# Kernel tuning notes

Hardware: AMD Instinct MI355X
Metric: run time of the kernel (lower is better)

## Reference

```python
import jax, jax.numpy as jnp
import numpy as np
import math

DIM = 512      # vMF embedding dim
B = 512        # batch
K = 10         # sample_size
C = 8192       # num_classes
L = 0.7        # kappa_confidence
T_REJ = 32     # fixed rejection-sampling tries (acceptance ~0.7 per try)


def _vmf_logc(k, dim=DIM):
    # Approximate log normalizer from the paper (approximate_logc=True path).
    nm14 = (dim - 1) / 4.0
    nm12 = (dim - 1) / 2.0
    np12 = (dim + 1) / 2.0
    sqrtm = jnp.sqrt(nm12 * nm12 + k * k)
    sqrtp = jnp.sqrt(np12 * np12 + k * k)
    return nm14 * (jnp.log(nm12 + sqrtm) + jnp.log(nm12 + sqrtp)) - 0.5 * (sqrtm + sqrtp)


def _split(params):
    # params layout: [log_probs(1), means(DIM), hidden_ik(1)] (single component).
    means = params[..., 1:1 + DIM]
    hidden_ik = params[..., -1]
    mu = means / jnp.linalg.norm(means, axis=-1, keepdims=True)
    kappa = 1.0 / jnp.exp(hidden_ik)  # positive(x) = exp(x) parametrization
    return mu, kappa


def _vmf_sample(key, mu, kappa, n):
    # Wood's algorithm, vectorized over (b, n) with fixed-count rejection.
    b, d = mu.shape
    kap = kappa[:, None]  # (b,1)
    bb = (-2.0 * kap + jnp.sqrt(4.0 * kap * kap + (d - 1) ** 2)) / (d - 1)
    x0 = (1.0 - bb) / (1.0 + bb)
    cc = kap * x0 + (d - 1) * jnp.log(1.0 - x0 * x0)
    kz, ku, kv = jax.random.split(key, 3)
    z = jax.random.beta(kz, (d - 1) / 2.0, (d - 1) / 2.0, (T_REJ, b, n))
    w = (1.0 - (1.0 + bb) * z) / (1.0 - (1.0 - bb) * z)  # (T,b,n)
    u = jax.random.uniform(ku, (T_REJ, b, n), minval=1e-10)
    acc = kap * w + (d - 1) * jnp.log(1.0 - x0 * w) - cc >= jnp.log(u)
    idx = jnp.argmax(acc, axis=0)  # first accepted try
    w_sel = jnp.take_along_axis(w, idx[None], axis=0)[0]  # (b,n)
    v = jax.random.normal(kv, (b, n, d))
    v = v - jnp.einsum('bnd,bd->bn', v, mu)[..., None] * mu[:, None, :]
    v = v / jnp.linalg.norm(v, axis=-1, keepdims=True)
    sin_t = jnp.sqrt(jnp.clip(1.0 - w_sel * w_sel, 0.0))
    return w_sel[..., None] * mu[:, None, :] + sin_t[..., None] * v  # (b,n,d)


def setup_inputs() -> dict:
    key = jax.random.key(0)
    kp, kw, kl = jax.random.split(key, 3)
    # Input distribution parameters: random means, hidden_ik ~ log(1/kappa) with realistic kappa.
    parameters = jax.random.normal(kp, (B, DIM + 2), dtype=jnp.float32)
    kappa0 = L / (1.0 - L * L) * (DIM - 1) / math.sqrt(DIM)  # ~31
    parameters = parameters.at[:, -1].set(0.1 * parameters[:, -1] - math.log(kappa0))
    # Class weight, built exactly as in __init__ (non-deterministic target).
    means = jax.random.normal(kw, (C, DIM), dtype=jnp.float32) * (L / (1.0 - L * L) * (DIM - 1) / math.sqrt(DIM))
    norm = jnp.linalg.norm(means, axis=-1, keepdims=True)
    hidden_ik = jnp.log(1.0 / norm)  # ipositive = log
    weight = jnp.concatenate([jnp.zeros((C, 1), jnp.float32), means, hidden_ik], axis=-1)
    log_scale = jnp.asarray(2.773, dtype=jnp.float32)
    labels = jax.random.randint(kl, (B,), 0, C)
    return {"parameters": parameters, "weight": weight, "log_scale": log_scale, "labels": labels}


def reference(parameters, weight, log_scale, labels):
    scale = jnp.exp(log_scale)
    mu_x, kappa_x = _split(parameters)   # (b,d), (b,)
    mu_w, kappa_w = _split(weight)       # (c,d), (c,)
    sample = _vmf_sample(jax.random.key(42), mu_x, kappa_x, K)  # (b,K,d)
    sample = sample / jnp.linalg.norm(sample, axis=-1, keepdims=True)
    # logmls(b,k,c): samples have concentration k1=scale; since all means are unit,
    # ||k1*m1 + k2*m2|| = sqrt(k1^2 + k2^2 + 2*k1*k2*cos) -> single GEMM over d.
    cos = jnp.einsum('bkd,cd->bkc', sample, mu_w)
    k1 = scale
    k2 = kappa_w
    kk = jnp.sqrt(k1 * k1 + k2 * k2 + 2.0 * k1 * (k2 * cos))  # (b,K,c)
    logmls = _vmf_logc(k1) + _vmf_logc(k2)[None, None, :] - _vmf_logc(kk)
    neg_logden = jax.scipy.special.logsumexp(logmls, axis=2) - _vmf_logc(scale)  # (b,K)
    neg_lognum = scale * jnp.einsum('bd,bd->b', mu_x, mu_w[labels])
    losses = neg_logden.mean(axis=1) - neg_lognum  # (b,)
    b = parameters.shape[0]
    logits = jnp.zeros((b, C), parameters.dtype).at[jnp.arange(b), labels].set(-losses)
    return logits
```

## Files before the change

### kernel.cpp

```cpp
#include <hip/hip_runtime.h>
#include <stdint.h>

#define DIMD 512
#define BATCH 512
#define KSAMP 10
#define NCLS 8192
#define TREJ 32

typedef float f32x4 __attribute__((ext_vector_type(4)));
typedef long l2 __attribute__((ext_vector_type(2)));

__device__ inline uint64_t sm64(uint64_t x) {
  x += 0x9E3779B97F4A7C15ull;
  x = (x ^ (x >> 30)) * 0xBF58476D1CE4E5B9ull;
  x = (x ^ (x >> 27)) * 0x94D049BB133111EBull;
  return x ^ (x >> 31);
}
__device__ inline float u01(uint32_t u) {
  return ((float)u + 0.5f) * 2.3283064365386963e-10f;
}
__device__ inline float normal_from(uint64_t r) {
  float u1 = u01((uint32_t)(r >> 32));
  float u2 = u01((uint32_t)r);
  return sqrtf(-2.0f * __logf(u1)) * __cosf(6.28318530718f * u2);
}
__device__ inline float gamma255(uint64_t& ctr) {
  const float dg = 255.1666667f;
  const float cg = 0.02086730f;
  for (int i = 0; i < 16; i++) {
    uint64_t r = sm64(ctr++);
    float x = normal_from(r);
    float t = fmaf(cg, x, 1.0f);
    if (t <= 0.0f) continue;
    float v3 = t * t * t;
    uint64_t r2 = sm64(ctr++);
    float u3 = u01((uint32_t)(r2 >> 32));
    if (__logf(u3) < 0.5f * x * x + dg * (1.0f - v3 + __logf(v3))) return dg * v3;
  }
  return dg;
}
__device__ inline float wave_sum(float v) {
  #pragma unroll
  for (int o = 32; o > 0; o >>= 1) v += __shfl_down(v, o, 64);
  return __shfl(v, 0, 64);
}
__device__ inline float vmf_logc(float k) {
  float k2 = k * k;
  float sm = sqrtf(65280.25f + k2);
  float sp = sqrtf(65792.25f + k2);
  return 127.75f * (__logf(255.5f + sm) + __logf(255.5f + sp)) - 0.5f * (sm + sp);
}
__device__ inline int2 pack_fp8x8(const float* v, float s) {
  int lo = 0, hi = 0;
  lo = __builtin_amdgcn_cvt_pk_fp8_f32(v[0] * s, v[1] * s, lo, false);
  lo = __builtin_amdgcn_cvt_pk_fp8_f32(v[2] * s, v[3] * s, lo, true);
  hi = __builtin_amdgcn_cvt_pk_fp8_f32(v[4] * s, v[5] * s, hi, false);
  hi = __builtin_amdgcn_cvt_pk_fp8_f32(v[6] * s, v[7] * s, hi, true);
  return make_int2(lo, hi);
}
__device__ inline int pk_off(int l) {
  return ((l >> 3) << 6) + ((l & 3) << 4) + (((l & 7) < 4) ? 0 : 8);
}
__device__ inline void sync_lds() {
  asm volatile("s_waitcnt lgkmcnt(0)\n\ts_barrier" ::: "memory");
}

__global__ __launch_bounds__(256) void prep_sample(const float* __restrict__ weight,
                                                   const float* __restrict__ params,
                                                   const float* __restrict__ lscale,
                                                   unsigned char* __restrict__ muW8,
                                                   float4* __restrict__ cparams,
                                                   float* __restrict__ rowsum,
                                                   float4* __restrict__ out4,
                                                   unsigned char* __restrict__ Sb8) {
  int blk = blockIdx.x, tid = threadIdx.x;
  int wave = tid >> 6, lane = tid & 63;
  if (blk < 2048) {
    out4[(size_t)blk * 512 + tid]       = make_float4(0.f, 0.f, 0.f, 0.f);
    out4[(size_t)blk * 512 + 256 + tid] = make_float4(0.f, 0.f, 0.f, 0.f);
    if (blk < 20) rowsum[blk * 256 + tid] = 0.0f;

    int c = blk * 4 + wave;
    const float* wr = weight + (size_t)c * (DIMD + 2) + 1;
    float v[8];
    float n2 = 0.0f;
    #pragma unroll
    for (int j = 0; j < 8; j++) { v[j] = wr[lane * 8 + j]; n2 += v[j] * v[j]; }
    n2 = wave_sum(n2);
    float inv = rsqrtf(n2) * 16.0f;
    int2 pk = pack_fp8x8(v, inv);
    *(int2*)(muW8 + (size_t)c * 512 + pk_off(lane)) = pk;

    float hik = wr[DIMD];
    float kw = __expf(-hik);
    float k1 = __expf(lscale[0]);
    float lcw = vmf_logc(kw);
    float A2 = fmaf(k1, k1, kw * kw);
    float B2 = 2.0f * k1 * kw;
    const float X0 = 0.9238795f, X1 = 0.3826834f;
    int l3 = lane & 3;
    float Xj = (l3 == 0) ? X0 : (l3 == 1) ? X1 : (l3 == 2) ? -X1 : -X0;
    float gj = lcw - vmf_logc(sqrtf(fmaf(B2, Xj, A2)));
    float g0 = __shfl(gj, 0, 64), g1 = __shfl(gj, 1, 64);
    float g2 = __shfl(gj, 2, 64), g3 = __shfl(gj, 3, 64);
    if (lane == 0) {
      float b0 = 0.25f * (g0 + g1 + g2 + g3);
      float b1 = 0.5f * (X0 * (g0 - g3) + X1 * (g1 - g2));
      float b2 = 0.5f * 0.7071068f * ((g0 + g3) - (g1 + g2));
      float b3 = 0.5f * (X1 * (g0 - g3) - X0 * (g1 - g2));
      const float L2E = 1.4426950409f;
      const float S1 = 1.0f / 256.0f;
      cparams[c] = make_float4((b0 - b2) * L2E, (b1 - 3.0f * b3) * L2E * S1,
                               (2.0f * b2) * L2E * S1 * S1,
                               (4.0f * b3) * L2E * S1 * S1 * S1);
    }
  } else {
    int row = (blk - 2048) * 4 + wave;
    int b = row / KSAMP;
    const float* pr = params + (size_t)b * (DIMD + 2) + 1;

    float mu[8];
    float n2 = 0.0f;
    #pragma unroll
    for (int j = 0; j < 8; j++) { mu[j] = pr[lane * 8 + j]; n2 += mu[j] * mu[j]; }
    n2 = wave_sum(n2);
    float invn = rsqrtf(n2);
    #pragma unroll
    for (int j = 0; j < 8; j++) mu[j] *= invn;

    float kap = __expf(-pr[DIMD]);
    float bb = (-2.0f * kap + sqrtf(fmaf(4.0f * kap, kap, 511.0f * 511.0f))) / 511.0f;
    float x0 = (1.0f - bb) / (1.0f + bb);
    float cc = kap * x0 + 511.0f * __logf(1.0f - x0 * x0);

    uint64_t ctr = (((uint64_t)(row + 1)) << 32) | ((uint64_t)lane << 8);
    float g1 = gamma255(ctr);
    float g2 = gamma255(ctr);
    float z = g1 / (g1 + g2);
    float wt = (1.0f - (1.0f + bb) * z) / (1.0f - (1.0f - bb) * z);
    uint64_t r = sm64(ctr++);
    float u = u01((uint32_t)(r >> 32));
    float lhs = kap * wt + 511.0f * __logf(1.0f - x0 * wt) - cc;
    bool acc = (lane < TREJ) && (lhs >= __logf(fmaxf(u, 1e-10f)));
    uint64_t mask = __ballot(acc);
    int sel = mask ? (__ffsll((unsigned long long)mask) - 1) : 0;
    float w = __shfl(wt, sel, 64);

    uint64_t cbase = (((uint64_t)(row + 1)) << 32) | 0x40000000ull;
    float v[8];
    #pragma unroll
    for (int j = 0; j < 8; j++) v[j] = normal_from(sm64(cbase + (uint64_t)(lane * 8 + j)));
    float d = 0.0f;
    #pragma unroll
    for (int j = 0; j < 8; j++) d += v[j] * mu[j];
    d = wave_sum(d);
    float t2 = 0.0f;
    #pragma unroll
    for (int j = 0; j < 8; j++) { v[j] -= d * mu[j]; t2 += v[j] * v[j]; }
    t2 = wave_sum(t2);
    float ivt = rsqrtf(t2);
    float st = sqrtf(fmaxf(0.0f, 1.0f - w * w)) * ivt;
    float sv[8];
    float s2 = 0.0f;
    #pragma unroll
    for (int j = 0; j < 8; j++) { sv[j] = fmaf(st, v[j], w * mu[j]); s2 += sv[j] * sv[j]; }
    s2 = wave_sum(s2);
    float is = rsqrtf(s2) * 16.0f;
    int2 pk = pack_fp8x8(sv, is);
    *(int2*)(Sb8 + (size_t)row * 512 + pk_off(lane)) = pk;
  }
}

__global__ __launch_bounds__(256, 3) void gemm_lse(const unsigned char* __restrict__ Sb8,
                                                   const unsigned char* __restrict__ Wb8,
                                                   const float4* __restrict__ cparams,
                                                   float* __restrict__ rowsum) {
  __shared__ __align__(16) unsigned char As[2][256 * 64];
  __shared__ __align__(16) unsigned char Bs[2][128 * 64];
  int tid = threadIdx.x;
  int lane = tid & 63, wave = tid >> 6;
  int tx = lane & 15, tz = lane >> 4;

  int id = blockIdx.x;
  int xcd = id & 7, lid = id >> 3;
  int c0 = (xcd * 8 + (lid & 7)) * 128;
  int r0 = (lid >> 3) * 256;

  int srow = lane >> 2;
  int slot = lane & 3;
  int kg = slot ^ ((srow >> 1) & 3);
  const unsigned char* gA[4];
  const unsigned char* gB[2];
  #pragma unroll
  for (int c = 0; c < 4; c++)
    gA[c] = Sb8 + (size_t)(r0 + (wave * 4 + c) * 16 + srow) * 512 + kg * 16;
  #pragma unroll
  for (int c = 0; c < 2; c++)
    gB[c] = Wb8 + (size_t)(c0 + (wave * 2 + c) * 16 + srow) * 512 + kg * 16;
  int ldsAo = (wave * 4) * 1024 + lane * 16;
  int ldsBo = (wave * 2) * 1024 + lane * 16;

  f32x4 acc[4][8];
  #pragma unroll
  for (int i = 0; i < 4; i++)
    #pragma unroll
    for (int j = 0; j < 8; j++) acc[i][j] = (f32x4){0.f, 0.f, 0.f, 0.f};

  int4 ar0[4], br0[2];
  int4 ar1[4], br1[2];

#define LOADCH(CI, AR, BR)                                   \
  { AR[0] = *(const int4*)(gA[0] + (CI) * 64);               \
    AR[1] = *(const int4*)(gA[1] + (CI) * 64);               \
    AR[2] = *(const int4*)(gA[2] + (CI) * 64);               \
    AR[3] = *(const int4*)(gA[3] + (CI) * 64);               \
    BR[0] = *(const int4*)(gB[0] + (CI) * 64);               \
    BR[1] = *(const int4*)(gB[1] + (CI) * 64); }

#define WRITELDS(P, AR, BR)                                  \
  { *(int4*)&As[P][ldsAo]        = AR[0];                    \
    *(int4*)&As[P][ldsAo + 1024] = AR[1];                    \
    *(int4*)&As[P][ldsAo + 2048] = AR[2];                    \
    *(int4*)&As[P][ldsAo + 3072] = AR[3];                    \
    *(int4*)&Bs[P][ldsBo]        = BR[0];                    \
    *(int4*)&Bs[P][ldsBo + 1024] = BR[1]; }

#define COMPUTE(P)                                                        \
  { l2 af[4];                                                             \
    int sA_ = tz ^ ((tx >> 1) & 3);                                       \
    _Pragma("unroll")                                                     \
    for (int mi = 0; mi < 4; mi++)                                        \
      af[mi] = *(const l2*)&As[P][(wave * 64 + mi * 16 + tx) * 64 + sA_ * 16]; \
    _Pragma("unroll")                                                     \
    for (int h = 0; h < 2; h++) {                                         \
      l2 bf[4];                                                           \
      _Pragma("unroll")                                                   \
      for (int ni = 0; ni < 4; ni++)                                      \
        bf[ni] = *(const l2*)&Bs[P][((h * 4 + ni) * 16 + tx) * 64 + sA_ * 16]; \
      __builtin_amdgcn_s_setprio(1);                                      \
      _Pragma("unroll")                                                   \
      for (int mi = 0; mi < 4; mi++)                                      \
        _Pragma("unroll")                                                 \
        for (int ni = 0; ni < 4; ni++)                                    \
          acc[mi][h * 4 + ni] = __builtin_amdgcn_mfma_f32_16x16x32_fp8_fp8(af[mi].x, bf[ni].x, acc[mi][h * 4 + ni], 0, 0, 0); \
      _Pragma("unroll")                                                   \
      for (int mi = 0; mi < 4; mi++)                                      \
        _Pragma("unroll")                                                 \
        for (int ni = 0; ni < 4; ni++)                                    \
          acc[mi][h * 4 + ni] = __builtin_amdgcn_mfma_f32_16x16x32_fp8_fp8(af[mi].y, bf[ni].y, acc[mi][h * 4 + ni], 0, 0, 0); \
      __builtin_amdgcn_s_setprio(0);                                      \
    } }

  LOADCH(0, ar0, br0);
  LOADCH(1, ar1, br1);
  WRITELDS(0, ar0, br0);
  sync_lds();

#define GITER_EVEN(IT)                                       \
  { if ((IT) + 2 < 8) LOADCH((IT) + 2, ar0, br0);            \
    COMPUTE(0);                                              \
    if ((IT) + 1 < 8) WRITELDS(1, ar1, br1);                 \
    if ((IT) < 7) sync_lds(); }

#define GITER_ODD(IT)                                        \
  { if ((IT) + 2 < 8) LOADCH((IT) + 2, ar1, br1);            \
    COMPUTE(1);                                              \
    if ((IT) + 1 < 8) WRITELDS(0, ar0, br0);                 \
    if ((IT) < 7) sync_lds(); }

  GITER_EVEN(0) GITER_ODD(1) GITER_EVEN(2) GITER_ODD(3)
  GITER_EVEN(4) GITER_ODD(5) GITER_EVEN(6) GITER_ODD(7)

  float4 cp[8];
  #pragma unroll
  for (int ni = 0; ni < 8; ni++) cp[ni] = cparams[c0 + ni * 16 + tx];

  #pragma unroll
  for (int mi = 0; mi < 4; mi++) {
    #pragma unroll
    for (int reg = 0; reg < 4; reg++) {
      float s = 0.0f;
      #pragma unroll
      for (int ni = 0; ni < 8; ni++) {
        float cv = acc[mi][ni][reg];
        float g = fmaf(fmaf(fmaf(cp[ni].w, cv, cp[ni].z), cv, cp[ni].y), cv, cp[ni].x);
        s += exp2f(g);
      }
      #pragma unroll
      for (int o = 1; o < 16; o <<= 1) s += __shfl_xor(s, o, 64);
      if (tx == 0)
        atomicAdd(&rowsum[r0 + wave * 64 + mi * 16 + tz * 4 + reg], s);
    }
  }
}

__global__ __launch_bounds__(64) void finalize_kernel(const float* __restrict__ params,
                                                      const float* __restrict__ weight,
                                                      const float* __restrict__ rowsum,
                                                      const int* __restrict__ labels,
                                                      const float* __restrict__ lscale,
                                                      float* __restrict__ out) {
  int b = blockIdx.x;
  int lane = threadIdx.x;
  int lab = labels[b];
  const float* pr = params + (size_t)b * (DIMD + 2) + 1;
  const float* wr = weight + (size_t)lab * (DIMD + 2) + 1;
  float nx = 0.0f, nw = 0.0f, d = 0.0f;
  #pragma unroll
  for (int j = 0; j < 8; j++) {
    float xv = pr[j * 64 + lane];
    float wv = wr[j * 64 + lane];
    nx += xv * xv; nw += wv * wv; d += xv * wv;
  }
  nx = wave_sum(nx); nw = wave_sum(nw); d = wave_sum(d);
  if (lane == 0) {
    float k1 = expf(lscale[0]);
    float acc = 0.0f;
    #pragma unroll
    for (int k = 0; k < KSAMP; k++) acc += __logf(rowsum[b * KSAMP + k]);
    float loss = acc * (1.0f / KSAMP) - k1 * d * rsqrtf(nx) * rsqrtf(nw);
    out[(size_t)b * NCLS + lab] = -loss;
  }
}

extern "C" void kernel_launch(void* const* d_in, const int* in_sizes, int n_in,
                              void* d_out, int out_size, void* d_ws, size_t ws_size,
                              hipStream_t stream) {
  const float* params = (const float*)d_in[0];
  const float* weight = (const float*)d_in[1];
  const float* lscale = (const float*)d_in[2];
  const int*   labels = (const int*)d_in[3];
  float* out = (float*)d_out;
  char* ws = (char*)d_ws;

  unsigned char* muW8    = (unsigned char*)(ws);
  unsigned char* Sb8     = (unsigned char*)(ws + 4194304);
  float4*        cparams = (float4*)(ws + 6815744);
  float*         rowsum  = (float*)(ws + 6946816);

  hipLaunchKernelGGL(prep_sample, dim3(2048 + BATCH * KSAMP / 4), dim3(256), 0, stream,
                     weight, params, lscale, muW8, cparams, rowsum, (float4*)out, Sb8);
  hipLaunchKernelGGL(gemm_lse, dim3((NCLS / 128) * (BATCH * KSAMP / 256)), dim3(256), 0, stream,
                     Sb8, muW8, cparams, rowsum);
  hipLaunchKernelGGL(finalize_kernel, dim3(BATCH), dim3(64), 0, stream,
                     params, weight, rowsum, labels, lscale, out);
}
```

Measured before the change: 166.6 us.

## Interleave global loads and LDS writes with MFMA phases using explicit barriers

Splits each GEMM main-loop iteration into four MFMA phases and interleaves the A/B global loads and LDS stores between them. sched_barrier fences and raw s_barrier instructions keep the compiler from reordering, in a ping-pong style schedule where waves alternate memory and MFMA work. It also lowers launch_bounds occupancy from 3 to 2 blocks per CU, giving more registers. The extra barriers per iteration add sync cost and rely on waves staying in lockstep, and the lower occupancy reduces latency hiding.

```diff
diff --git a/kernel.cpp b/kernel.cpp
--- a/kernel.cpp
+++ b/kernel.cpp
@@ -171,7 +171,7 @@
   }
 }
 
-__global__ __launch_bounds__(256, 3) void gemm_lse(const unsigned char* __restrict__ Sb8,
+__global__ __launch_bounds__(256, 2) void gemm_lse(const unsigned char* __restrict__ Sb8,
                                                    const unsigned char* __restrict__ Wb8,
                                                    const float4* __restrict__ cparams,
                                                    float* __restrict__ rowsum) {
@@ -209,67 +209,86 @@
   int4 ar0[4], br0[2];
   int4 ar1[4], br1[2];
 
-#define LOADCH(CI, AR, BR)                                   \
+#define LOADCH_A(CI, AR)                                     \
   { AR[0] = *(const int4*)(gA[0] + (CI) * 64);               \
     AR[1] = *(const int4*)(gA[1] + (CI) * 64);               \
     AR[2] = *(const int4*)(gA[2] + (CI) * 64);               \
-    AR[3] = *(const int4*)(gA[3] + (CI) * 64);               \
-    BR[0] = *(const int4*)(gB[0] + (CI) * 64);               \
+    AR[3] = *(const int4*)(gA[3] + (CI) * 64); }
+
+#define LOADCH_B(CI, BR)                                     \
+  { BR[0] = *(const int4*)(gB[0] + (CI) * 64);               \
     BR[1] = *(const int4*)(gB[1] + (CI) * 64); }
 
-#define WRITELDS(P, AR, BR)                                  \
+#define WRITELDS_A(P, AR)                                    \
   { *(int4*)&As[P][ldsAo]        = AR[0];                    \
     *(int4*)&As[P][ldsAo + 1024] = AR[1];                    \
     *(int4*)&As[P][ldsAo + 2048] = AR[2];                    \
-    *(int4*)&As[P][ldsAo + 3072] = AR[3];                    \
-    *(int4*)&Bs[P][ldsBo]        = BR[0];                    \
+    *(int4*)&As[P][ldsAo + 3072] = AR[3]; }
+
+#define WRITELDS_B(P, BR)                                    \
+  { *(int4*)&Bs[P][ldsBo]        = BR[0];                    \
     *(int4*)&Bs[P][ldsBo + 1024] = BR[1]; }
 
-#define COMPUTE(P)                                                        \
-  { l2 af[4];                                                             \
-    int sA_ = tz ^ ((tx >> 1) & 3);                                       \
+#define READ_AF(P)                                                        \
+  _Pragma("unroll")                                                       \
+  for (int mi = 0; mi < 4; mi++)                                          \
+    af[mi] = *(const l2*)&As[P][(wave * 64 + mi * 16 + tx) * 64 + sA_ * 16];
+
+#define READ_BF(P, H)                                                     \
+  _Pragma("unroll")                                                       \
+  for (int ni = 0; ni < 4; ni++)                                          \
+    bf[ni] = *(const l2*)&Bs[P][(((H) * 4 + ni) * 16 + tx) * 64 + sA_ * 16];
+
+#define MFMA16(H, COMP)                                                   \
+  _Pragma("unroll")                                                       \
+  for (int mi = 0; mi < 4; mi++)                                          \
     _Pragma("unroll")                                                     \
-    for (int mi = 0; mi < 4; mi++)                                        \
-      af[mi] = *(const l2*)&As[P][(wave * 64 + mi * 16 + tx) * 64 + sA_ * 16]; \
-    _Pragma("unroll")                                                     \
-    for (int h = 0; h < 2; h++) {                                         \
-      l2 bf[4];                                                           \
-      _Pragma("unroll")                                                   \
-      for (int ni = 0; ni < 4; ni++)                                      \
-        bf[ni] = *(const l2*)&Bs[P][((h * 4 + ni) * 16 + tx) * 64 + sA_ * 16]; \
-      __builtin_amdgcn_s_setprio(1);                                      \
-      _Pragma("unroll")                                                   \
-      for (int mi = 0; mi < 4; mi++)                                      \
-        _Pragma("unroll")                                                 \
-        for (int ni = 0; ni < 4; ni++)                                    \
-          acc[mi][h * 4 + ni] = __builtin_amdgcn_mfma_f32_16x16x32_fp8_fp8(af[mi].x, bf[ni].x, acc[mi][h * 4 + ni], 0, 0, 0); \
-      _Pragma("unroll")                                                   \
-      for (int mi = 0; mi < 4; mi++)                                      \
-        _Pragma("unroll")                                                 \
-        for (int ni = 0; ni < 4; ni++)                                    \
-          acc[mi][h * 4 + ni] = __builtin_amdgcn_mfma_f32_16x16x32_fp8_fp8(af[mi].y, bf[ni].y, acc[mi][h * 4 + ni], 0, 0, 0); \
-      __builtin_amdgcn_s_setprio(0);                                      \
-    } }
-
-  LOADCH(0, ar0, br0);
-  LOADCH(1, ar1, br1);
-  WRITELDS(0, ar0, br0);
+    for (int ni = 0; ni < 4; ni++)                                        \
+      acc[mi][(H) * 4 + ni] = __builtin_amdgcn_mfma_f32_16x16x32_fp8_fp8( \
+          af[mi].COMP, bf[ni].COMP, acc[mi][(H) * 4 + ni], 0, 0, 0);
+
+#define PH_BEGIN                                             \
+  __builtin_amdgcn_sched_barrier(0);                         \
+  asm volatile("s_barrier\n\ts_waitcnt lgkmcnt(0)" ::: "memory"); \
+  __builtin_amdgcn_sched_barrier(0);                         \
+  __builtin_amdgcn_s_setprio(1);
+
+#define PH_END                                               \
+  __builtin_amdgcn_s_setprio(0);                             \
+  __builtin_amdgcn_sched_barrier(0);                         \
+  asm volatile("s_barrier" ::: "memory");                    \
+  __builtin_amdgcn_sched_barrier(0);
+
+#define GITER(P, Q, IT, ARL, BRL, ARW, BRW)                  \
+  { l2 af[4]; l2 bf[4];                                      \
+    int sA_ = tz ^ ((tx >> 1) & 3);                          \
+    READ_AF(P) READ_BF(P, 0)                                 \
+    if ((IT) + 2 < 8) LOADCH_A((IT) + 2, ARL);               \
+    PH_BEGIN MFMA16(0, x) PH_END                             \
+    if ((IT) + 2 < 8) LOADCH_B((IT) + 2, BRL);               \
+    PH_BEGIN MFMA16(0, y) PH_END                             \
+    READ_BF(P, 1)                                            \
+    if ((IT) + 1 < 8) WRITELDS_A(Q, ARW);                    \
+    PH_BEGIN MFMA16(1, x) PH_END                             \
+    if ((IT) + 1 < 8) WRITELDS_B(Q, BRW);                    \
+    PH_BEGIN MFMA16(1, y)                                    \
+    __builtin_amdgcn_s_setprio(0);                           \
+    __builtin_amdgcn_sched_barrier(0);                       \
+    if ((IT) < 7) sync_lds(); }
+
+  LOADCH_A(0, ar0); LOADCH_B(0, br0);
+  LOADCH_A(1, ar1); LOADCH_B(1, br1);
+  WRITELDS_A(0, ar0); WRITELDS_B(0, br0);
   sync_lds();
 
-#define GITER_EVEN(IT)                                       \
-  { if ((IT) + 2 < 8) LOADCH((IT) + 2, ar0, br0);            \
-    COMPUTE(0);                                              \
-    if ((IT) + 1 < 8) WRITELDS(1, ar1, br1);                 \
-    if ((IT) < 7) sync_lds(); }
-
-#define GITER_ODD(IT)                                        \
-  { if ((IT) + 2 < 8) LOADCH((IT) + 2, ar1, br1);            \
-    COMPUTE(1);                                              \
-    if ((IT) + 1 < 8) WRITELDS(0, ar0, br0);                 \
-    if ((IT) < 7) sync_lds(); }
-
-  GITER_EVEN(0) GITER_ODD(1) GITER_EVEN(2) GITER_ODD(3)
-  GITER_EVEN(4) GITER_ODD(5) GITER_EVEN(6) GITER_ODD(7)
+  GITER(0, 1, 0, ar0, br0, ar1, br1)
+  GITER(1, 0, 1, ar1, br1, ar0, br0)
+  GITER(0, 1, 2, ar0, br0, ar1, br1)
+  GITER(1, 0, 3, ar1, br1, ar0, br0)
+  GITER(0, 1, 4, ar0, br0, ar1, br1)
+  GITER(1, 0, 5, ar1, br1, ar0, br0)
+  GITER(0, 1, 6, ar0, br0, ar1, br1)
+  GITER(1, 0, 7, ar1, br1, ar0, br0)
 
   float4 cp[8];
   #pragma unroll
```

Result: faster. 144.8 us (-13.1%).

## Stage GEMM tiles via direct global-to-LDS loads instead of register staging

Applied to the files above, without the earlier changes.

The fp8 GEMM main loop now uses global_load_lds to copy A/B tiles straight into shared memory, replacing the register round-trip (global load to VGPRs, then LDS write). The double-buffer schedule is rebuilt around vmcnt waits and barriers, and the s_setprio hints are removed. Launch bounds drop from 3 to 2 blocks per SIMD, which gives each thread more registers but may lower occupancy. Staging into LDS without going through registers is meant to cut VGPR pressure and instruction count, at the cost of tighter barrier coupling between loads and compute.

```diff
diff --git a/kernel.cpp b/kernel.cpp
--- a/kernel.cpp
+++ b/kernel.cpp
@@ -61,8 +61,10 @@
 __device__ inline int pk_off(int l) {
   return ((l >> 3) << 6) + ((l & 3) << 4) + (((l & 7) < 4) ? 0 : 8);
 }
-__device__ inline void sync_lds() {
-  asm volatile("s_waitcnt lgkmcnt(0)\n\ts_barrier" ::: "memory");
+__device__ inline void gld16(const unsigned char* g, unsigned char* l) {
+  __builtin_amdgcn_global_load_lds(
+      (const __attribute__((address_space(1))) unsigned int*)g,
+      (__attribute__((address_space(3))) unsigned int*)l, 16, 0, 0);
 }
 
 __global__ __launch_bounds__(256) void prep_sample(const float* __restrict__ weight,
@@ -171,7 +173,7 @@
   }
 }
 
-__global__ __launch_bounds__(256, 3) void gemm_lse(const unsigned char* __restrict__ Sb8,
+__global__ __launch_bounds__(256, 2) void gemm_lse(const unsigned char* __restrict__ Sb8,
                                                    const unsigned char* __restrict__ Wb8,
                                                    const float4* __restrict__ cparams,
                                                    float* __restrict__ rowsum) {
@@ -197,8 +199,8 @@
   #pragma unroll
   for (int c = 0; c < 2; c++)
     gB[c] = Wb8 + (size_t)(c0 + (wave * 2 + c) * 16 + srow) * 512 + kg * 16;
-  int ldsAo = (wave * 4) * 1024 + lane * 16;
-  int ldsBo = (wave * 2) * 1024 + lane * 16;
+  int ldsA0 = (wave * 4) * 1024;
+  int ldsB0 = (wave * 2) * 1024;
 
   f32x4 acc[4][8];
   #pragma unroll
@@ -206,24 +208,13 @@
     #pragma unroll
     for (int j = 0; j < 8; j++) acc[i][j] = (f32x4){0.f, 0.f, 0.f, 0.f};
 
-  int4 ar0[4], br0[2];
-  int4 ar1[4], br1[2];
-
-#define LOADCH(CI, AR, BR)                                   \
-  { AR[0] = *(const int4*)(gA[0] + (CI) * 64);               \
-    AR[1] = *(const int4*)(gA[1] + (CI) * 64);               \
-    AR[2] = *(const int4*)(gA[2] + (CI) * 64);               \
-    AR[3] = *(const int4*)(gA[3] + (CI) * 64);               \
-    BR[0] = *(const int4*)(gB[0] + (CI) * 64);               \
-    BR[1] = *(const int4*)(gB[1] + (CI) * 64); }
-
-#define WRITELDS(P, AR, BR)                                  \
-  { *(int4*)&As[P][ldsAo]        = AR[0];                    \
-    *(int4*)&As[P][ldsAo + 1024] = AR[1];                    \
-    *(int4*)&As[P][ldsAo + 2048] = AR[2];                    \
-    *(int4*)&As[P][ldsAo + 3072] = AR[3];                    \
-    *(int4*)&Bs[P][ldsBo]        = BR[0];                    \
-    *(int4*)&Bs[P][ldsBo + 1024] = BR[1]; }
+#define STAGE(P, CI)                                         \
+  { gld16(gA[0] + (CI) * 64, &As[P][ldsA0]);                 \
+    gld16(gA[1] + (CI) * 64, &As[P][ldsA0 + 1024]);          \
+    gld16(gA[2] + (CI) * 64, &As[P][ldsA0 + 2048]);          \
+    gld16(gA[3] + (CI) * 64, &As[P][ldsA0 + 3072]);          \
+    gld16(gB[0] + (CI) * 64, &Bs[P][ldsB0]);                 \
+    gld16(gB[1] + (CI) * 64, &Bs[P][ldsB0 + 1024]); }
 
 #define COMPUTE(P)                                                        \
   { l2 af[4];                                                             \
@@ -237,7 +228,6 @@
       _Pragma("unroll")                                                   \
       for (int ni = 0; ni < 4; ni++)                                      \
         bf[ni] = *(const l2*)&Bs[P][((h * 4 + ni) * 16 + tx) * 64 + sA_ * 16]; \
-      __builtin_amdgcn_s_setprio(1);                                      \
       _Pragma("unroll")                                                   \
       for (int mi = 0; mi < 4; mi++)                                      \
         _Pragma("unroll")                                                 \
@@ -248,28 +238,28 @@
         _Pragma("unroll")                                                 \
         for (int ni = 0; ni < 4; ni++)                                    \
           acc[mi][h * 4 + ni] = __builtin_amdgcn_mfma_f32_16x16x32_fp8_fp8(af[mi].y, bf[ni].y, acc[mi][h * 4 + ni], 0, 0, 0); \
-      __builtin_amdgcn_s_setprio(0);                                      \
     } }
 
-  LOADCH(0, ar0, br0);
-  LOADCH(1, ar1, br1);
-  WRITELDS(0, ar0, br0);
-  sync_lds();
-
-#define GITER_EVEN(IT)                                       \
-  { if ((IT) + 2 < 8) LOADCH((IT) + 2, ar0, br0);            \
-    COMPUTE(0);                                              \
-    if ((IT) + 1 < 8) WRITELDS(1, ar1, br1);                 \
-    if ((IT) < 7) sync_lds(); }
-
-#define GITER_ODD(IT)                                        \
-  { if ((IT) + 2 < 8) LOADCH((IT) + 2, ar1, br1);            \
-    COMPUTE(1);                                              \
-    if ((IT) + 1 < 8) WRITELDS(0, ar0, br0);                 \
-    if ((IT) < 7) sync_lds(); }
-
-  GITER_EVEN(0) GITER_ODD(1) GITER_EVEN(2) GITER_ODD(3)
-  GITER_EVEN(4) GITER_ODD(5) GITER_EVEN(6) GITER_ODD(7)
+  STAGE(0, 0);
+  STAGE(1, 1);
+  asm volatile("s_waitcnt vmcnt(6)" ::: "memory");
+  __builtin_amdgcn_s_barrier();
+
+#define GITER(P, IT)                                                      \
+  { COMPUTE(P);                                                           \
+    if ((IT) < 7) {                                                       \
+      asm volatile("s_waitcnt lgkmcnt(0)\n\ts_barrier" ::: "memory");     \
+      if ((IT) + 2 < 8) {                                                 \
+        STAGE(P, (IT) + 2);                                               \
+        asm volatile("s_waitcnt vmcnt(6)" ::: "memory");                  \
+      } else {                                                            \
+        asm volatile("s_waitcnt vmcnt(0)" ::: "memory");                  \
+      }                                                                   \
+      __builtin_amdgcn_s_barrier();                                       \
+    } }
+
+  GITER(0, 0) GITER(1, 1) GITER(0, 2) GITER(1, 3)
+  GITER(0, 4) GITER(1, 5) GITER(0, 6) GITER(1, 7)
 
   float4 cp[8];
   #pragma unroll
```

Result: faster. 139.8 us (-16.1%).
